# Kernel tuning notes

Measured on AMD Instinct MI355X. Metric: run time of the kernel, lower is better.

Reference implementation:

```python
import jax, jax.numpy as jnp
from jax import lax
import numpy as np

V, D, L, E = 32000, 256, 4, 4
B, S = 1, 4096  # B must be 1: AstroNorm's buffer update/broadcast only works for batch==1
SIG = float(1.0 / (1.0 + np.exp(-0.15)))        # sigmoid(init_sparsity=0.15), static (int() detaches)
K_GATE = max(1, int(S * SIG))                    # tokens kept by sparsity gate
K_EXP = max(1, int(0.8 * E))                     # int(sparsity_constraint * num_experts) = 3


def setup_inputs() -> dict:
    key = jax.random.key(0)
    ks = jax.random.split(key, 8)
    s = 0.02
    return {
        "tokens": jax.random.randint(ks[0], (B, S), 0, V),
        "emb": jax.random.normal(ks[1], (V, D)) * s,
        "buffers": jax.random.normal(ks[2], (L, D)) * 0.1,   # AstroNorm buffer per layer
        "decays": jnp.full((L,), 0.95),                       # AstroNorm decay per layer
        "gate_w": jax.random.normal(ks[3], (L, D)) * s,       # context_gate (Linear(dim,1,bias=False))
        "gating_W": jax.random.normal(ks[4], (L, E, D)) * s,  # expert router
        "gating_b": jnp.zeros((L, E)),
        "exp_W": jax.random.normal(ks[5], (L, E, D, D)) * s,  # per-expert Linear(dim,dim)
        "exp_b": jnp.zeros((L, E, D)),
        "ln_g": jnp.ones((D,)),
        "ln_b": jnp.zeros((D,)),
        "head_W": jax.random.normal(ks[6], (V, D)) * s,
        "head_b": jnp.zeros((V,)),
    }


def _forward(tokens, emb, buffers, decays, gate_w, gating_W, gating_b,
             exp_W, exp_b, ln_g, ln_b, head_W, head_b):
    x = emb[tokens]  # [B,S,D]
    for l in range(L):
        # ---- AstroNorm: stats over sequence dim (dim=1), detached as in torch ----
        mu = lax.stop_gradient(jnp.mean(x, axis=1, keepdims=True))           # [B,1,D]
        var = lax.stop_gradient(jnp.var(x, axis=1, keepdims=True, ddof=1))   # unbiased var
        new_buf = decays[l] * buffers[l] + (1.0 - decays[l]) * mu.squeeze()  # [D] (B==1)
        x = jnp.where(jnp.abs(x - mu) > jnp.abs(new_buf), mu, x) / jnp.sqrt(var + 1e-6)
        # ---- DynamicSparsityGate: keep tokens strictly above k-th score ----
        scores = jnp.einsum('bsd,d->bs', x, gate_w[l])
        thr = lax.top_k(scores, K_GATE)[0][:, -1:]           # k-th largest per row
        x = x * (scores > thr).astype(x.dtype)[..., None]
        # ---- SparseExpert: top-K_EXP experts per token, masked accumulation ----
        gs = jnp.einsum('bsd,ed->bse', x, gating_W[l]) + gating_b[l]
        idx = lax.top_k(gs, K_EXP)[1]                                    # [B,S,k]
        emask = (jax.nn.one_hot(idx, E).sum(-2) > 0).astype(x.dtype)     # [B,S,E]
        ys = jnp.einsum('bsd,eod->bseo', x, exp_W[l]) + exp_b[l]         # all-expert outputs
        x = jnp.einsum('bse,bseo->bso', emask, ys)
    # ---- LayerNorm (biased var, eps=1e-5) + vocab head ----
    mu = jnp.mean(x, axis=-1, keepdims=True)
    v = jnp.var(x, axis=-1, keepdims=True)
    x = (x - mu) / jnp.sqrt(v + 1e-5) * ln_g + ln_b
    return jnp.einsum('bsd,vd->bsv', x, head_W) + head_b


def reference(tokens, emb, buffers, decays, gate_w, gating_W, gating_b,
              exp_W, exp_b, ln_g, ln_b, head_W, head_b):
    return _forward(tokens, emb, buffers, decays, gate_w, gating_W, gating_b,
                    exp_W, exp_b, ln_g, ln_b, head_W, head_b)
```

## Files before the change

### kernel.cpp

```cpp
#include <hip/hip_runtime.h>
#include <hip/hip_bf16.h>
#include <math.h>

#define V 32000
#define D 256
#define L 4
#define E 4
#define S 4096
#define K_GATE 2201
#define NE 1024
#define NCH 64
#define SCHUNK 64
#define CTS 136


typedef __hip_bfloat16 bf16;
typedef __attribute__((ext_vector_type(8))) short bf16x8;
typedef __attribute__((ext_vector_type(4))) float f32x4;

__device__ __forceinline__ float loadf(const void* p, size_t i, int bf) {
    if (bf) return __bfloat162float(((const bf16*)p)[i]);
    return ((const float*)p)[i];
}
__device__ __forceinline__ float us2f(unsigned short u) {
    return __uint_as_float((unsigned)u << 16);
}

#define GLDS16(g, l)                                                            \
    __builtin_amdgcn_global_load_lds(                                           \
        (const __attribute__((address_space(1))) unsigned int*)(g),             \
        (__attribute__((address_space(3))) unsigned int*)(l), 16, 0, 0)

__device__ __forceinline__ void stage_tile(const bf16* __restrict__ src, int rowStride,
                                           short* lds, int t, int k0) {
    int w = t >> 6, l = t & 63;
    #pragma unroll
    for (int i = 0; i < 2; i++) {
        int chunk = (w * 2 + i) * 64 + l;
        int row = chunk >> 2;
        int c8 = (chunk & 3) ^ ((row >> 1) & 3);
        const bf16* g = src + (size_t)row * rowStride + k0 + c8 * 8;
        GLDS16(g, (char*)lds + (size_t)(w * 2 + i) * 1024);
    }
}

__device__ __forceinline__ bf16x8 frag_ld(const short* lds, int row, int quad) {
    return *(const bf16x8*)&lds[row * 32 + ((quad ^ ((row >> 1) & 3)) << 3)];
}

__global__ void k_detect(const void* __restrict__ emb, int* __restrict__ flag) {
    const unsigned short* h = (const unsigned short*)emb;
    int cnt = 0;
    for (int i = 0; i < 128; i += 2) {
        int e = (h[i] >> 7) & 0xFF;
        if (e >= 100 && e <= 130) cnt++;
    }
    *flag = (cnt >= 32) ? 1 : 0;
}

__global__ void k_wcast(const void* __restrict__ W, const int* __restrict__ bfp,
                        bf16* __restrict__ Wb) {
    if (*bfp) return;
    size_t idx = ((size_t)blockIdx.x * 256 + threadIdx.x) * 4;
    float4 v = *(const float4*)((const float*)W + idx);
    Wb[idx + 0] = __float2bfloat16(v.x);
    Wb[idx + 1] = __float2bfloat16(v.y);
    Wb[idx + 2] = __float2bfloat16(v.z);
    Wb[idx + 3] = __float2bfloat16(v.w);
}

__global__ void k_embed(const int* __restrict__ tok, const void* __restrict__ emb,
                        const int* __restrict__ bfp, float* __restrict__ x) {
    int s = blockIdx.x, d = threadIdx.x;
    int bf = *bfp;
    int t = tok[s];
    x[s * D + d] = loadf(emb, (size_t)t * D + d, bf);
}

__global__ void k_stats_part(const float* __restrict__ x, float* __restrict__ psum,
                             float* __restrict__ psq) {
    int b = blockIdx.x;
    int t = threadIdx.x;
    float s = 0.f, q = 0.f;
    int s0 = b * SCHUNK;
    #pragma unroll 4
    for (int i = 0; i < SCHUNK; i++) {
        float v = x[(size_t)(s0 + i) * D + t];
        s += v; q += v * v;
    }
    psum[b * D + t] = s;
    psq[b * D + t] = q;
}

__global__ void k_stats_fin(const float* __restrict__ psum, const float* __restrict__ psq,
                            const void* __restrict__ buffers, const void* __restrict__ decays,
                            const int* __restrict__ bfp, int l,
                            float* __restrict__ mu, float* __restrict__ rstd,
                            float* __restrict__ absnb) {
    int t = threadIdx.x;
    int bf = *bfp;
    float s = 0.f, q = 0.f;
    for (int b = 0; b < NCH; b++) { s += psum[b * D + t]; q += psq[b * D + t]; }
    float m = s / (float)S;
    float var = (q - (float)S * m * m) / (float)(S - 1);
    float dec = loadf(decays, l, bf);
    float nb = dec * loadf(buffers, l * D + t, bf) + (1.f - dec) * m;
    mu[t] = m;
    rstd[t] = rsqrtf(var + 1e-6f);
    absnb[t] = fabsf(nb);
}

__global__ void k_norm_score(float* __restrict__ x, const float* __restrict__ mu,
                             const float* __restrict__ rstd, const float* __restrict__ absnb,
                             const void* __restrict__ gate_w, const int* __restrict__ bfp,
                             int l, float* __restrict__ scores) {
    int t = threadIdx.x, w = t >> 6, ln = t & 63;
    int s = blockIdx.x * 4 + w;
    int bf = *bfp;
    float part = 0.f;
    #pragma unroll
    for (int j = 0; j < 4; j++) {
        int f = ln + j * 64;
        float m = mu[f];
        float v = x[(size_t)s * D + f];
        float xv = (fabsf(v - m) > absnb[f]) ? m : v;
        xv *= rstd[f];
        x[(size_t)s * D + f] = xv;
        part += xv * loadf(gate_w, l * D + f, bf);
    }
    #pragma unroll
    for (int m2 = 1; m2 < 64; m2 <<= 1) part += __shfl_xor(part, m2, 64);
    if (ln == 0) scores[s] = part;
}

__global__ void k_thr(const float* __restrict__ scores, float* __restrict__ thr) {
    __shared__ unsigned keys[S];
    __shared__ unsigned hist[256];
    __shared__ unsigned sh_pref, sh_rank, sh_bucket;
    int t = threadIdx.x;
    #pragma unroll
    for (int i = 0; i < 4; i++) {
        int idx = i * 1024 + t;
        unsigned u = __float_as_uint(scores[idx]);
        keys[idx] = (u & 0x80000000u) ? ~u : (u | 0x80000000u);
    }
    if (t == 0) { sh_pref = 0u; sh_rank = S - K_GATE; }
    __syncthreads();
    for (int shift = 24; shift >= 0; shift -= 8) {
        if (t < 256) hist[t] = 0u;
        __syncthreads();
        unsigned pref = sh_pref, r = sh_rank;
        unsigned pmask = (shift == 24) ? 0u : (0xFFFFFFFFu << (shift + 8));
        #pragma unroll
        for (int i = 0; i < 4; i++) {
            unsigned k = keys[i * 1024 + t];
            if ((k & pmask) == pref) atomicAdd(&hist[(k >> shift) & 0xFF], 1u);
        }
        __syncthreads();
        if (t < 64) {
            unsigned h[4];
            unsigned loc = 0u;
            #pragma unroll
            for (int j = 0; j < 4; j++) { h[j] = hist[t * 4 + j]; loc += h[j]; }
            unsigned pre = loc;
            #pragma unroll
            for (int off = 1; off < 64; off <<= 1) {
                unsigned u2 = __shfl_up(pre, off, 64);
                if (t >= off) pre += u2;
            }
            unsigned base = pre - loc;
            if (r >= base && r < pre) {
                unsigned rr = r - base;
                int bsel = -1;
                #pragma unroll
                for (int j = 0; j < 4; j++) {
                    if (bsel < 0) {
                        if (rr < h[j]) bsel = j;
                        else rr -= h[j];
                    }
                }
                sh_bucket = (unsigned)(t * 4 + bsel);
                sh_rank = rr;
            }
        }
        __syncthreads();
        if (t == 0) sh_pref = pref | (sh_bucket << shift);
        __syncthreads();
    }
    if (t == 0) {
        unsigned k = sh_pref;
        unsigned u = (k & 0x80000000u) ? (k ^ 0x80000000u) : ~k;
        thr[0] = __uint_as_float(u);
    }
}

#define EBM 128
#define EBN 128
#define EBK 32
__global__ __launch_bounds__(256) void k_egemm(const float* __restrict__ x,
                                               const float* __restrict__ scores,
                                               const float* __restrict__ thr,
                                               const void* __restrict__ exp_W,
                                               const int* __restrict__ bfp, int l,
                                               float* __restrict__ Y) {
    __shared__ float As[EBK][EBM + 4];
    __shared__ float Bs[EBK][EBN + 4];
    __shared__ float kp[EBM];
    int bf = *bfp;
    int bn = blockIdx.x * EBN;
    int bm = blockIdx.y * EBM;
    int t = threadIdx.x;
    int tm = (t >> 4) * 8;
    int tn = (t & 15) * 8;
    if (t < EBM) kp[t] = (scores[bm + t] > thr[0]) ? 1.f : 0.f;
    __syncthreads();
    const unsigned short* Wb16 = (const unsigned short*)exp_W;
    const float* Wf32 = (const float*)exp_W;
    size_t wbase = (size_t)l * NE * D;
    float acc[8][8] = {};
    for (int k0 = 0; k0 < D; k0 += EBK) {
        #pragma unroll
        for (int i = 0; i < 4; i++) {
            int chunk = i * 256 + t;
            int m = chunk >> 3, c4 = chunk & 7;
            float4 v = *(const float4*)&x[(size_t)(bm + m) * D + k0 + c4 * 4];
            float kk = kp[m];
            As[c4 * 4 + 0][m] = v.x * kk;
            As[c4 * 4 + 1][m] = v.y * kk;
            As[c4 * 4 + 2][m] = v.z * kk;
            As[c4 * 4 + 3][m] = v.w * kk;
        }
        if (bf) {
            #pragma unroll
            for (int i = 0; i < 2; i++) {
                int chunk = i * 256 + t;
                int n = chunk >> 2, c8 = chunk & 3;
                const unsigned short* src = Wb16 + wbase + (size_t)(bn + n) * D + k0 + c8 * 8;
                ushort4 v0 = *(const ushort4*)src;
                ushort4 v1 = *(const ushort4*)(src + 4);
                Bs[c8 * 8 + 0][n] = us2f(v0.x);
                Bs[c8 * 8 + 1][n] = us2f(v0.y);
                Bs[c8 * 8 + 2][n] = us2f(v0.z);
                Bs[c8 * 8 + 3][n] = us2f(v0.w);
                Bs[c8 * 8 + 4][n] = us2f(v1.x);
                Bs[c8 * 8 + 5][n] = us2f(v1.y);
                Bs[c8 * 8 + 6][n] = us2f(v1.z);
                Bs[c8 * 8 + 7][n] = us2f(v1.w);
            }
        } else {
            #pragma unroll
            for (int i = 0; i < 4; i++) {
                int chunk = i * 256 + t;
                int n = chunk >> 3, c4 = chunk & 7;
                float4 v = *(const float4*)&Wf32[wbase + (size_t)(bn + n) * D + k0 + c4 * 4];
                Bs[c4 * 4 + 0][n] = v.x;
                Bs[c4 * 4 + 1][n] = v.y;
                Bs[c4 * 4 + 2][n] = v.z;
                Bs[c4 * 4 + 3][n] = v.w;
            }
        }
        __syncthreads();
        #pragma unroll 4
        for (int k = 0; k < EBK; k++) {
            float a[8], b[8];
            *(float4*)&a[0] = *(const float4*)&As[k][tm];
            *(float4*)&a[4] = *(const float4*)&As[k][tm + 4];
            *(float4*)&b[0] = *(const float4*)&Bs[k][tn];
            *(float4*)&b[4] = *(const float4*)&Bs[k][tn + 4];
            #pragma unroll
            for (int i = 0; i < 8; i++)
                #pragma unroll
                for (int j = 0; j < 8; j++)
                    acc[i][j] += a[i] * b[j];
        }
        __syncthreads();
    }
    #pragma unroll
    for (int i = 0; i < 8; i++) {
        float4 o0 = { acc[i][0], acc[i][1], acc[i][2], acc[i][3] };
        float4 o1 = { acc[i][4], acc[i][5], acc[i][6], acc[i][7] };
        float* dst = &Y[(size_t)(bm + tm + i) * NE + bn + tn];
        *(float4*)dst = o0;
        *(float4*)(dst + 4) = o1;
    }
}

__global__ void k_comb(const float* __restrict__ x, const float* __restrict__ scores,
                       const float* __restrict__ thr,
                       const void* __restrict__ gating_W, const void* __restrict__ gating_b,
                       const float* __restrict__ Y, const void* __restrict__ exp_b,
                       const int* __restrict__ bfp, int l, float* __restrict__ xo) {
    int t = threadIdx.x, w = t >> 6, ln = t & 63;
    int s = blockIdx.x * 4 + w;
    int bf = *bfp;
    float keep = (scores[s] > thr[0]) ? 1.f : 0.f;
    float xv[4];
    #pragma unroll
    for (int j = 0; j < 4; j++)
        xv[j] = x[(size_t)s * D + ln + j * 64] * keep;
    float gs[E];
    #pragma unroll
    for (int e = 0; e < E; e++) {
        float p = 0.f;
        #pragma unroll
        for (int j = 0; j < 4; j++)
            p += xv[j] * loadf(gating_W, (size_t)(l * E + e) * D + ln + j * 64, bf);
        #pragma unroll
        for (int m2 = 1; m2 < 64; m2 <<= 1) p += __shfl_xor(p, m2, 64);
        gs[e] = p + loadf(gating_b, l * E + e, bf);
    }
    int mi = 0;
    if (ln == 0) {
        float mv = gs[0];
        #pragma unroll
        for (int e = 1; e < E; e++) if (gs[e] <= mv) { mv = gs[e]; mi = e; }
    }
    int excl = __shfl(mi, 0, 64);
    #pragma unroll
    for (int j = 0; j < 4; j++) {
        int f = ln + j * 64;
        float a = 0.f;
        for (int e = 0; e < E; e++) {
            if (e == excl) continue;
            a += Y[(size_t)s * NE + e * D + f] + loadf(exp_b, (size_t)(l * E + e) * D + f, bf);
        }
        xo[(size_t)s * D + f] = a;
    }
}

__global__ void k_ln(const float* __restrict__ x, const void* __restrict__ g,
                     const void* __restrict__ b, const int* __restrict__ bfp,
                     bf16* __restrict__ xnb) {
    int t = threadIdx.x, w = t >> 6, ln = t & 63;
    int s = blockIdx.x * 4 + w;
    int bf = *bfp;
    float vv[4];
    float sum = 0.f, sq = 0.f;
    #pragma unroll
    for (int j = 0; j < 4; j++) {
        float v = x[(size_t)s * D + ln + j * 64];
        vv[j] = v; sum += v; sq += v * v;
    }
    #pragma unroll
    for (int m2 = 1; m2 < 64; m2 <<= 1) {
        sum += __shfl_xor(sum, m2, 64);
        sq  += __shfl_xor(sq, m2, 64);
    }
    float m = sum / (float)D;
    float var = sq / (float)D - m * m;
    float r = rsqrtf(var + 1e-5f);
    #pragma unroll
    for (int j = 0; j < 4; j++) {
        int f = ln + j * 64;
        xnb[(size_t)s * D + f] = __float2bfloat16((vv[j] - m) * r * loadf(g, f, bf)
                                                  + loadf(b, f, bf));
    }
}

__global__ __launch_bounds__(256) void k_head_mfma(const bf16* __restrict__ xnb,
                                                   const void* __restrict__ head_W_raw,
                                                   const bf16* __restrict__ Wb,
                                                   const void* __restrict__ bias,
                                                   const int* __restrict__ bfp,
                                                   void* __restrict__ out) {
    __shared__ __align__(16) char smem[128 * CTS * 2];
    short* At = (short*)smem;
    short* Bt = (short*)(smem + 8192);
    short* Ct = (short*)smem;
    int bf = *bfp;
    const bf16* Wsrc = bf ? (const bf16*)head_W_raw : Wb;
    int bs = blockIdx.x * 128;
    int bv = blockIdx.y * 128;
    int t = threadIdx.x;
    int wave = t >> 6, lane = t & 63;
    int wm = (wave >> 1) * 64, wn = (wave & 1) * 64;
    int quad = lane >> 4, l16 = lane & 15;

    f32x4 acc[4][4] = {};
    for (int k0 = 0; k0 < D; k0 += 32) {
        stage_tile(xnb + (size_t)bs * D, D, At, t, k0);
        stage_tile(Wsrc + (size_t)bv * D, D, Bt, t, k0);
        __syncthreads();
        bf16x8 af[4], bfg[4];
        #pragma unroll
        for (int i = 0; i < 4; i++) af[i]  = frag_ld(At, wm + i * 16 + l16, quad);
        #pragma unroll
        for (int j = 0; j < 4; j++) bfg[j] = frag_ld(Bt, wn + j * 16 + l16, quad);
        #pragma unroll
        for (int i = 0; i < 4; i++)
            #pragma unroll
            for (int j = 0; j < 4; j++)
                acc[i][j] = __builtin_amdgcn_mfma_f32_16x16x32_bf16(af[i], bfg[j], acc[i][j], 0, 0, 0);
        __syncthreads();
    }
    if (bf) {
        #pragma unroll
        for (int j = 0; j < 4; j++) {
            int colL = wn + j * 16 + l16;
            float bb = __bfloat162float(((const bf16*)bias)[bv + colL]);
            #pragma unroll
            for (int i = 0; i < 4; i++) {
                int rowL = wm + i * 16 + quad * 4;
                #pragma unroll
                for (int rg = 0; rg < 4; rg++) {
                    bf16 hv = __float2bfloat16(acc[i][j][rg] + bb);
                    Ct[(rowL + rg) * CTS + colL] = *(short*)&hv;
                }
            }
        }
        __syncthreads();
        bf16* ob = (bf16*)out;
        #pragma unroll
        for (int k = 0; k < 8; k++) {
            int cc = k * 256 + t;
            int row = cc >> 4, c16 = cc & 15;
            bf16x8 v = *(const bf16x8*)&Ct[row * CTS + c16 * 8];
            *(bf16x8*)(ob + (size_t)(bs + row) * V + bv + c16 * 8) = v;
        }
    } else {
        float* of = (float*)out;
        #pragma unroll
        for (int j = 0; j < 4; j++) {
            int col = bv + wn + j * 16 + l16;
            float bb = loadf(bias, col, bf);
            #pragma unroll
            for (int i = 0; i < 4; i++) {
                int row0 = bs + wm + i * 16 + quad * 4;
                #pragma unroll
                for (int rg = 0; rg < 4; rg++)
                    of[(size_t)(row0 + rg) * V + col] = acc[i][j][rg] + bb;
            }
        }
    }
}

extern "C" void kernel_launch(void* const* d_in, const int* in_sizes, int n_in,
                              void* d_out, int out_size, void* d_ws, size_t ws_size,
                              hipStream_t stream) {
    const int*  tokens   = (const int*)d_in[0];
    const void* emb      = d_in[1];
    const void* buffers  = d_in[2];
    const void* decays   = d_in[3];
    const void* gate_w   = d_in[4];
    const void* gating_W = d_in[5];
    const void* gating_b = d_in[6];
    const void* exp_W    = d_in[7];
    const void* exp_b    = d_in[8];
    const void* ln_g     = d_in[9];
    const void* ln_b     = d_in[10];
    const void* head_W   = d_in[11];
    const void* head_b   = d_in[12];

    char* p = (char*)d_ws;
    bf16* Wb    = (bf16*)p;             p += (size_t)V * D * 2;
    bf16* xnb   = (bf16*)p;             p += (size_t)S * D * 2;
    float* xA   = (float*)p;            p += (size_t)S * D * 4;
    float* xB   = (float*)p;            p += (size_t)S * D * 4;
    float* Y    = (float*)p;            p += (size_t)S * NE * 4;
    float* psum = (float*)p;            p += (size_t)NCH * D * 4;
    float* psq  = (float*)p;            p += (size_t)NCH * D * 4;
    float* scores = (float*)p;          p += (size_t)S * 4;
    float* mu   = (float*)p;            p += D * 4;
    float* rstd = (float*)p;            p += D * 4;
    float* absnb = (float*)p;           p += D * 4;
    float* thr  = (float*)p;            p += 16;
    int* flag   = (int*)p;              p += 16;

    k_detect<<<1, 1, 0, stream>>>(emb, flag);
    k_wcast<<<(V * D) / 1024, 256, 0, stream>>>(head_W, flag, Wb);
    k_embed<<<S, D, 0, stream>>>(tokens, emb, flag, xA);

    float* xc = xA;
    float* xo = xB;
    for (int l = 0; l < L; l++) {
        k_stats_part<<<NCH, 256, 0, stream>>>(xc, psum, psq);
        k_stats_fin<<<1, 256, 0, stream>>>(psum, psq, buffers, decays, flag, l, mu, rstd, absnb);
        k_norm_score<<<S / 4, 256, 0, stream>>>(xc, mu, rstd, absnb, gate_w, flag, l, scores);
        k_thr<<<1, 1024, 0, stream>>>(scores, thr);
        dim3 ge(NE / EBN, S / EBM);
        k_egemm<<<ge, 256, 0, stream>>>(xc, scores, thr, exp_W, flag, l, Y);
        k_comb<<<S / 4, 256, 0, stream>>>(xc, scores, thr, gating_W, gating_b, Y,
                                          exp_b, flag, l, xo);
        float* tmp = xc; xc = xo; xo = tmp;
    }
    k_ln<<<S / 4, 256, 0, stream>>>(xc, ln_g, ln_b, flag, xnb);
    dim3 gh(S / 128, V / 128);
    k_head_mfma<<<gh, 256, 0, stream>>>(xnb, head_W, Wb, head_b, flag, d_out);
}
```

Before: 993.0 us.

## Fuse expert GEMM with masked combine, split routing, fold stats finalize into norm

Removes the S x 1024 intermediate Y buffer by computing all four expert outputs per tile in one kernel and summing the three selected experts in the epilogue with bias. Routing (gating top-3 exclusion) moves to a small separate kernel that writes the excluded expert index per token. The single-block stats finalize kernel is merged into the norm/score kernel, where each block recomputes the mean, rstd and buffer threshold redundantly into shared memory. The cost is smaller GEMM tiles (32x64 per block, 2x4 per thread per expert) with lower arithmetic intensity and more shared memory for four weight tiles.

```diff
diff --git a/kernel.cpp b/kernel.cpp
--- a/kernel.cpp
+++ b/kernel.cpp
@@ -8,7 +8,6 @@
 #define E 4
 #define S 4096
 #define K_GATE 2201
-#define NE 1024
 #define NCH 64
 #define SCHUNK 64
 #define CTS 136
@@ -92,39 +91,36 @@
     psq[b * D + t] = q;
 }
 
-__global__ void k_stats_fin(const float* __restrict__ psum, const float* __restrict__ psq,
-                            const void* __restrict__ buffers, const void* __restrict__ decays,
-                            const int* __restrict__ bfp, int l,
-                            float* __restrict__ mu, float* __restrict__ rstd,
-                            float* __restrict__ absnb) {
-    int t = threadIdx.x;
-    int bf = *bfp;
-    float s = 0.f, q = 0.f;
-    for (int b = 0; b < NCH; b++) { s += psum[b * D + t]; q += psq[b * D + t]; }
-    float m = s / (float)S;
-    float var = (q - (float)S * m * m) / (float)(S - 1);
-    float dec = loadf(decays, l, bf);
-    float nb = dec * loadf(buffers, l * D + t, bf) + (1.f - dec) * m;
-    mu[t] = m;
-    rstd[t] = rsqrtf(var + 1e-6f);
-    absnb[t] = fabsf(nb);
-}
-
-__global__ void k_norm_score(float* __restrict__ x, const float* __restrict__ mu,
-                             const float* __restrict__ rstd, const float* __restrict__ absnb,
+__global__ void k_norm_score(float* __restrict__ x, const float* __restrict__ psum,
+                             const float* __restrict__ psq,
+                             const void* __restrict__ buffers, const void* __restrict__ decays,
                              const void* __restrict__ gate_w, const int* __restrict__ bfp,
                              int l, float* __restrict__ scores) {
+    __shared__ float mu_s[D], rstd_s[D], absnb_s[D];
     int t = threadIdx.x, w = t >> 6, ln = t & 63;
+    int bf = *bfp;
+    {
+        float s = 0.f, q = 0.f;
+        #pragma unroll 8
+        for (int b = 0; b < NCH; b++) { s += psum[b * D + t]; q += psq[b * D + t]; }
+        float m = s / (float)S;
+        float var = (q - (float)S * m * m) / (float)(S - 1);
+        float dec = loadf(decays, l, bf);
+        float nb = dec * loadf(buffers, l * D + t, bf) + (1.f - dec) * m;
+        mu_s[t] = m;
+        rstd_s[t] = rsqrtf(var + 1e-6f);
+        absnb_s[t] = fabsf(nb);
+    }
+    __syncthreads();
     int s = blockIdx.x * 4 + w;
-    int bf = *bfp;
     float part = 0.f;
     #pragma unroll
     for (int j = 0; j < 4; j++) {
         int f = ln + j * 64;
-        float m = mu[f];
+        float m = mu_s[f];
         float v = x[(size_t)s * D + f];
-        float xv = (fabsf(v - m) > absnb[f]) ? m : v;
-        xv *= rstd[f];
+        float xv = (fabsf(v - m) > absnb_s[f]) ? m : v;
+        xv *= rstd_s[f];
         x[(size_t)s * D + f] = xv;
         part += xv * loadf(gate_w, l * D + f, bf);
     }
@@ -194,35 +190,71 @@
     }
 }
 
-#define EBM 128
-#define EBN 128
-#define EBK 32
-__global__ __launch_bounds__(256) void k_egemm(const float* __restrict__ x,
-                                               const float* __restrict__ scores,
-                                               const float* __restrict__ thr,
-                                               const void* __restrict__ exp_W,
-                                               const int* __restrict__ bfp, int l,
-                                               float* __restrict__ Y) {
-    __shared__ float As[EBK][EBM + 4];
-    __shared__ float Bs[EBK][EBN + 4];
-    __shared__ float kp[EBM];
-    int bf = *bfp;
-    int bn = blockIdx.x * EBN;
-    int bm = blockIdx.y * EBM;
+__global__ void k_route(const float* __restrict__ x, const float* __restrict__ scores,
+                        const float* __restrict__ thr,
+                        const void* __restrict__ gating_W, const void* __restrict__ gating_b,
+                        const int* __restrict__ bfp, int l, int* __restrict__ excl) {
+    int t = threadIdx.x, w = t >> 6, ln = t & 63;
+    int s = blockIdx.x * 4 + w;
+    int bf = *bfp;
+    float keep = (scores[s] > thr[0]) ? 1.f : 0.f;
+    float xv[4];
+    #pragma unroll
+    for (int j = 0; j < 4; j++)
+        xv[j] = x[(size_t)s * D + ln + j * 64] * keep;
+    float gs[E];
+    #pragma unroll
+    for (int e = 0; e < E; e++) {
+        float p = 0.f;
+        #pragma unroll
+        for (int j = 0; j < 4; j++)
+            p += xv[j] * loadf(gating_W, (size_t)(l * E + e) * D + ln + j * 64, bf);
+        #pragma unroll
+        for (int m2 = 1; m2 < 64; m2 <<= 1) p += __shfl_xor(p, m2, 64);
+        gs[e] = p + loadf(gating_b, l * E + e, bf);
+    }
+    if (ln == 0) {
+        int mi = 0;
+        float mv = gs[0];
+        #pragma unroll
+        for (int e = 1; e < E; e++) if (gs[e] <= mv) { mv = gs[e]; mi = e; }
+        excl[s] = mi;
+    }
+}
+
+#define MBM 32
+#define MBN 64
+#define MBK 32
+__global__ __launch_bounds__(256) void k_moe(const float* __restrict__ x,
+                                             const float* __restrict__ scores,
+                                             const float* __restrict__ thr,
+                                             const int* __restrict__ excl,
+                                             const void* __restrict__ exp_W,
+                                             const void* __restrict__ exp_b,
+                                             const int* __restrict__ bfp, int l,
+                                             float* __restrict__ xo) {
+    __shared__ float As[MBK][MBM + 2];
+    __shared__ float Bs[E][MBK][MBN + 4];
+    __shared__ float kp[MBM];
+    __shared__ int exs[MBM];
+    int bf = *bfp;
+    int bnf = blockIdx.x * MBN;
+    int bm = blockIdx.y * MBM;
     int t = threadIdx.x;
-    int tm = (t >> 4) * 8;
-    int tn = (t & 15) * 8;
-    if (t < EBM) kp[t] = (scores[bm + t] > thr[0]) ? 1.f : 0.f;
+    int tm = (t >> 4) * 2;
+    int tn = (t & 15) * 4;
+    if (t < MBM) {
+        kp[t] = (scores[bm + t] > thr[0]) ? 1.f : 0.f;
+        exs[t] = excl[bm + t];
+    }
     __syncthreads();
     const unsigned short* Wb16 = (const unsigned short*)exp_W;
     const float* Wf32 = (const float*)exp_W;
-    size_t wbase = (size_t)l * NE * D;
-    float acc[8][8] = {};
-    for (int k0 = 0; k0 < D; k0 += EBK) {
-        #pragma unroll
-        for (int i = 0; i < 4; i++) {
-            int chunk = i * 256 + t;
-            int m = chunk >> 3, c4 = chunk & 7;
+    size_t wbase = (size_t)l * E * D * D;
+    float acc[E][2][4] = {};
+    for (int k0 = 0; k0 < D; k0 += MBK) {
+        {
+            int m = t >> 3, c4 = t & 7;
             float4 v = *(const float4*)&x[(size_t)(bm + m) * D + k0 + c4 * 4];
             float kk = kp[m];
             As[c4 * 4 + 0][m] = v.x * kk;
@@ -230,101 +262,74 @@
             As[c4 * 4 + 2][m] = v.z * kk;
             As[c4 * 4 + 3][m] = v.w * kk;
         }
-        if (bf) {
-            #pragma unroll
-            for (int i = 0; i < 2; i++) {
-                int chunk = i * 256 + t;
-                int n = chunk >> 2, c8 = chunk & 3;
-                const unsigned short* src = Wb16 + wbase + (size_t)(bn + n) * D + k0 + c8 * 8;
-                ushort4 v0 = *(const ushort4*)src;
-                ushort4 v1 = *(const ushort4*)(src + 4);
-                Bs[c8 * 8 + 0][n] = us2f(v0.x);
-                Bs[c8 * 8 + 1][n] = us2f(v0.y);
-                Bs[c8 * 8 + 2][n] = us2f(v0.z);
-                Bs[c8 * 8 + 3][n] = us2f(v0.w);
-                Bs[c8 * 8 + 4][n] = us2f(v1.x);
-                Bs[c8 * 8 + 5][n] = us2f(v1.y);
-                Bs[c8 * 8 + 6][n] = us2f(v1.z);
-                Bs[c8 * 8 + 7][n] = us2f(v1.w);
-            }
-        } else {
-            #pragma unroll
-            for (int i = 0; i < 4; i++) {
-                int chunk = i * 256 + t;
-                int n = chunk >> 3, c4 = chunk & 7;
-                float4 v = *(const float4*)&Wf32[wbase + (size_t)(bn + n) * D + k0 + c4 * 4];
-                Bs[c4 * 4 + 0][n] = v.x;
-                Bs[c4 * 4 + 1][n] = v.y;
-                Bs[c4 * 4 + 2][n] = v.z;
-                Bs[c4 * 4 + 3][n] = v.w;
+        int n = t >> 2, c8 = t & 3;
+        #pragma unroll
+        for (int e = 0; e < E; e++) {
+            size_t roff = wbase + ((size_t)e * D + bnf + n) * D + k0 + c8 * 8;
+            if (bf) {
+                ushort4 v0 = *(const ushort4*)(Wb16 + roff);
+                ushort4 v1 = *(const ushort4*)(Wb16 + roff + 4);
+                Bs[e][c8 * 8 + 0][n] = us2f(v0.x);
+                Bs[e][c8 * 8 + 1][n] = us2f(v0.y);
+                Bs[e][c8 * 8 + 2][n] = us2f(v0.z);
+                Bs[e][c8 * 8 + 3][n] = us2f(v0.w);
+                Bs[e][c8 * 8 + 4][n] = us2f(v1.x);
+                Bs[e][c8 * 8 + 5][n] = us2f(v1.y);
+                Bs[e][c8 * 8 + 6][n] = us2f(v1.z);
+                Bs[e][c8 * 8 + 7][n] = us2f(v1.w);
+            } else {
+                float4 v0 = *(const float4*)(Wf32 + roff);
+                float4 v1 = *(const float4*)(Wf32 + roff + 4);
+                Bs[e][c8 * 8 + 0][n] = v0.x;
+                Bs[e][c8 * 8 + 1][n] = v0.y;
+                Bs[e][c8 * 8 + 2][n] = v0.z;
+                Bs[e][c8 * 8 + 3][n] = v0.w;
+                Bs[e][c8 * 8 + 4][n] = v1.x;
+                Bs[e][c8 * 8 + 5][n] = v1.y;
+                Bs[e][c8 * 8 + 6][n] = v1.z;
+                Bs[e][c8 * 8 + 7][n] = v1.w;
             }
         }
         __syncthreads();
         #pragma unroll 4
-        for (int k = 0; k < EBK; k++) {
-            float a[8], b[8];
-            *(float4*)&a[0] = *(const float4*)&As[k][tm];
-            *(float4*)&a[4] = *(const float4*)&As[k][tm + 4];
-            *(float4*)&b[0] = *(const float4*)&Bs[k][tn];
-            *(float4*)&b[4] = *(const float4*)&Bs[k][tn + 4];
-            #pragma unroll
-            for (int i = 0; i < 8; i++)
+        for (int k = 0; k < MBK; k++) {
+            float a0 = As[k][tm];
+            float a1 = As[k][tm + 1];
+            #pragma unroll
+            for (int e = 0; e < E; e++) {
+                float4 b = *(const float4*)&Bs[e][k][tn];
+                acc[e][0][0] += a0 * b.x;
+                acc[e][0][1] += a0 * b.y;
+                acc[e][0][2] += a0 * b.z;
+                acc[e][0][3] += a0 * b.w;
+                acc[e][1][0] += a1 * b.x;
+                acc[e][1][1] += a1 * b.y;
+                acc[e][1][2] += a1 * b.z;
+                acc[e][1][3] += a1 * b.w;
+            }
+        }
+        __syncthreads();
+    }
+    float fin[2][4] = {};
+    #pragma unroll
+    for (int e = 0; e < E; e++) {
+        float be[4];
+        #pragma unroll
+        for (int j = 0; j < 4; j++)
+            be[j] = loadf(exp_b, (size_t)(l * E + e) * D + bnf + tn + j, bf);
+        #pragma unroll
+        for (int i = 0; i < 2; i++) {
+            if (exs[tm + i] != e) {
                 #pragma unroll
-                for (int j = 0; j < 8; j++)
-                    acc[i][j] += a[i] * b[j];
-        }
-        __syncthreads();
-    }
-    #pragma unroll
-    for (int i = 0; i < 8; i++) {
-        float4 o0 = { acc[i][0], acc[i][1], acc[i][2], acc[i][3] };
-        float4 o1 = { acc[i][4], acc[i][5], acc[i][6], acc[i][7] };
-        float* dst = &Y[(size_t)(bm + tm + i) * NE + bn + tn];
-        *(float4*)dst = o0;
-        *(float4*)(dst + 4) = o1;
-    }
-}
-
-__global__ void k_comb(const float* __restrict__ x, const float* __restrict__ scores,
-                       const float* __restrict__ thr,
-                       const void* __restrict__ gating_W, const void* __restrict__ gating_b,
-                       const float* __restrict__ Y, const void* __restrict__ exp_b,
-                       const int* __restrict__ bfp, int l, float* __restrict__ xo) {
-    int t = threadIdx.x, w = t >> 6, ln = t & 63;
-    int s = blockIdx.x * 4 + w;
-    int bf = *bfp;
-    float keep = (scores[s] > thr[0]) ? 1.f : 0.f;
-    float xv[4];
-    #pragma unroll
-    for (int j = 0; j < 4; j++)
-        xv[j] = x[(size_t)s * D + ln + j * 64] * keep;
-    float gs[E];
-    #pragma unroll
-    for (int e = 0; e < E; e++) {
-        float p = 0.f;
-        #pragma unroll
-        for (int j = 0; j < 4; j++)
-            p += xv[j] * loadf(gating_W, (size_t)(l * E + e) * D + ln + j * 64, bf);
-        #pragma unroll
-        for (int m2 = 1; m2 < 64; m2 <<= 1) p += __shfl_xor(p, m2, 64);
-        gs[e] = p + loadf(gating_b, l * E + e, bf);
-    }
-    int mi = 0;
-    if (ln == 0) {
-        float mv = gs[0];
-        #pragma unroll
-        for (int e = 1; e < E; e++) if (gs[e] <= mv) { mv = gs[e]; mi = e; }
-    }
-    int excl = __shfl(mi, 0, 64);
-    #pragma unroll
-    for (int j = 0; j < 4; j++) {
-        int f = ln + j * 64;
-        float a = 0.f;
-        for (int e = 0; e < E; e++) {
-            if (e == excl) continue;
-            a += Y[(size_t)s * NE + e * D + f] + loadf(exp_b, (size_t)(l * E + e) * D + f, bf);
-        }
-        xo[(size_t)s * D + f] = a;
+                for (int j = 0; j < 4; j++)
+                    fin[i][j] += acc[e][i][j] + be[j];
+            }
+        }
+    }
+    #pragma unroll
+    for (int i = 0; i < 2; i++) {
+        float4 o = { fin[i][0], fin[i][1], fin[i][2], fin[i][3] };
+        *(float4*)&xo[(size_t)(bm + tm + i) * D + bnf + tn] = o;
     }
 }
 
@@ -456,13 +461,10 @@
     bf16* xnb   = (bf16*)p;             p += (size_t)S * D * 2;
     float* xA   = (float*)p;            p += (size_t)S * D * 4;
     float* xB   = (float*)p;            p += (size_t)S * D * 4;
-    float* Y    = (float*)p;            p += (size_t)S * NE * 4;
     float* psum = (float*)p;            p += (size_t)NCH * D * 4;
     float* psq  = (float*)p;            p += (size_t)NCH * D * 4;
     float* scores = (float*)p;          p += (size_t)S * 4;
-    float* mu   = (float*)p;            p += D * 4;
-    float* rstd = (float*)p;            p += D * 4;
-    float* absnb = (float*)p;           p += D * 4;
+    int* excl   = (int*)p;              p += (size_t)S * 4;
     float* thr  = (float*)p;            p += 16;
     int* flag   = (int*)p;              p += 16;
 
@@ -474,13 +476,13 @@
     float* xo = xB;
     for (int l = 0; l < L; l++) {
         k_stats_part<<<NCH, 256, 0, stream>>>(xc, psum, psq);
-        k_stats_fin<<<1, 256, 0, stream>>>(psum, psq, buffers, decays, flag, l, mu, rstd, absnb);
-        k_norm_score<<<S / 4, 256, 0, stream>>>(xc, mu, rstd, absnb, gate_w, flag, l, scores);
+        k_norm_score<<<S / 4, 256, 0, stream>>>(xc, psum, psq, buffers, decays,
+                                                gate_w, flag, l, scores);
         k_thr<<<1, 1024, 0, stream>>>(scores, thr);
-        dim3 ge(NE / EBN, S / EBM);
-        k_egemm<<<ge, 256, 0, stream>>>(xc, scores, thr, exp_W, flag, l, Y);
-        k_comb<<<S / 4, 256, 0, stream>>>(xc, scores, thr, gating_W, gating_b, Y,
-                                          exp_b, flag, l, xo);
+        k_route<<<S / 4, 256, 0, stream>>>(xc, scores, thr, gating_W, gating_b,
+                                           flag, l, excl);
+        dim3 gm(D / MBN, S / MBM);
+        k_moe<<<gm, 256, 0, stream>>>(xc, scores, thr, excl, exp_W, exp_b, flag, l, xo);
         float* tmp = xc; xc = xo; xo = tmp;
     }
     k_ln<<<S / 4, 256, 0, stream>>>(xc, ln_g, ln_b, flag, xnb);
```

Result: no change. 989.8 us (-0.3%).
